# Optimization experiments

Hardware: AMD Instinct MI355X
Metric: run time of the kernel (lower is better)

The kernel has to match this reference:

```python
import math
import jax, jax.numpy as jnp
import numpy as np

DIM = 2048
NUM_HEADS = 16
HEAD_DIM = DIM // NUM_HEADS
BASE = 10000.0


def _rope(x):
    # x: [B, S, H, D]; non-interleaved (chunk-half) rotary embedding
    S, D = x.shape[1], x.shape[-1]
    inv_freq = 1.0 / (BASE ** (jnp.arange(0, D, 2, dtype=jnp.float32) / D))
    t = jnp.arange(S, dtype=jnp.float32)
    freqs = jnp.outer(t, inv_freq)  # [S, D/2]
    cos = jnp.cos(freqs)[None, :, None, :].astype(x.dtype)
    sin = jnp.sin(freqs)[None, :, None, :].astype(x.dtype)
    x1, x2 = jnp.split(x, 2, axis=-1)
    return jnp.concatenate([x1 * cos - x2 * sin, x1 * sin + x2 * cos], axis=-1)


def setup_inputs() -> dict:
    key = jax.random.key(0)
    kx, kq, kk, kv, ko = jax.random.split(key, 5)
    x = jax.random.normal(kx, (2, 2048, DIM), dtype=jnp.float32)
    scale = 0.02
    Wq = jax.random.normal(kq, (DIM, DIM), dtype=jnp.float32) * scale
    Wk = jax.random.normal(kk, (DIM, DIM), dtype=jnp.float32) * scale
    Wv = jax.random.normal(kv, (DIM, DIM), dtype=jnp.float32) * scale
    Wo = jax.random.normal(ko, (DIM, DIM), dtype=jnp.float32) * scale
    return {"x": x, "Wq": Wq, "Wk": Wk, "Wv": Wv, "Wo": Wo}


def reference(x, Wq, Wk, Wv, Wo):
    B, S, _ = x.shape
    # nn.Linear(bias=False): y = x @ W.T
    q = (x @ Wq.T).reshape(B, S, NUM_HEADS, HEAD_DIM)
    k = (x @ Wk.T).reshape(B, S, NUM_HEADS, HEAD_DIM)
    v = (x @ Wv.T).reshape(B, S, NUM_HEADS, HEAD_DIM)
    q = _rope(q)
    k = _rope(k)
    scale = 1.0 / math.sqrt(HEAD_DIM)
    # causal attention, [B,H,S,S] scores
    scores = jnp.einsum("bqhd,bkhd->bhqk", q, k) * scale
    causal = jnp.tril(jnp.ones((S, S), dtype=bool))
    scores = jnp.where(causal[None, None], scores, jnp.finfo(scores.dtype).min)
    attn = jax.nn.softmax(scores, axis=-1)
    out = jnp.einsum("bhqk,bkhd->bqhd", attn, v).reshape(B, S, DIM)
    return out @ Wo.T
```

## Files before the change

### kernel.cpp

```cpp
#include <hip/hip_runtime.h>

typedef unsigned short u16;
typedef __attribute__((ext_vector_type(8))) short short8;
typedef __attribute__((ext_vector_type(4))) float f32x4;
typedef __attribute__((ext_vector_type(4))) int i32x4;

__device__ __forceinline__ float bf2f(u16 u) {
  union { unsigned u; float f; } v; v.u = ((unsigned)u) << 16; return v.f;
}
__device__ __forceinline__ u16 f2bf(float f) {
  union { float f; unsigned u; } v; v.f = f;
  unsigned r = (v.u + 0x7FFFu + ((v.u >> 16) & 1u)) >> 16;
  return (u16)r;
}
__device__ __forceinline__ float flushv(float t, float sentinel) {
  if (t != t || fabsf(t) > 3.0e38f) return sentinel;
  return t;
}
__device__ __forceinline__ short8 ld8f(const float* p) {
  const float4 f0 = *(const float4*)p;
  const float4 f1 = *(const float4*)(p + 4);
  short8 r;
  r[0] = (short)f2bf(f0.x); r[1] = (short)f2bf(f0.y);
  r[2] = (short)f2bf(f0.z); r[3] = (short)f2bf(f0.w);
  r[4] = (short)f2bf(f1.x); r[5] = (short)f2bf(f1.y);
  r[6] = (short)f2bf(f1.z); r[7] = (short)f2bf(f1.w);
  return r;
}

__device__ __forceinline__ void gl16(const u16* g, u16* l) {
  __builtin_amdgcn_global_load_lds(
      (const __attribute__((address_space(1))) void*)g,
      (__attribute__((address_space(3))) void*)l, 16, 0, 0);
}

#define VWAIT(N) asm volatile("s_waitcnt vmcnt(" #N ")" ::: "memory")
#define SBAR() do { __builtin_amdgcn_sched_barrier(0); \
                    __builtin_amdgcn_s_barrier(); \
                    __builtin_amdgcn_sched_barrier(0); } while (0)

__global__ __launch_bounds__(256) void cvt_all(
    const float* __restrict__ x,
    const float* __restrict__ Wq, const float* __restrict__ Wk,
    const float* __restrict__ Wv, const float* __restrict__ Wo,
    u16* __restrict__ xb, u16* __restrict__ wqb, u16* __restrict__ wkb,
    u16* __restrict__ wvb, u16* __restrict__ wob)
{
  const int bid = blockIdx.x;
  const float* s; u16* d; long t;
  if (bid < 8192) {
    const int which = bid >> 11;
    t = (long)(bid & 2047) * 256 + threadIdx.x;
    if (which == 0)      { s = Wq; d = wqb; }
    else if (which == 1) { s = Wk; d = wkb; }
    else if (which == 2) { s = Wv; d = wvb; }
    else                 { s = Wo; d = wob; }
  } else {
    s = x; d = xb;
    t = (long)(bid - 8192) * 256 + threadIdx.x;
  }
  *(short8*)&d[t * 8] = ld8f(s + t * 8);
}

template <bool OF>
__device__ __forceinline__ void gemm_core(
    const u16* __restrict__ Ap, const u16* __restrict__ Bp,
    void* __restrict__ O, int m0, int n0, int N, float sentinel)
{
  __shared__ __align__(16) u16 As[2][128 * 32];
  __shared__ __align__(16) u16 Bs[2][128 * 32];
  constexpr int K = 2048;

  const int tid  = threadIdx.x;
  const int wave = tid >> 6;
  const int lane = tid & 63;
  const int quad = lane >> 4;
  const int l15  = lane & 15;

  const int wm = (wave >> 1) * 64;
  const int wn = (wave & 1) * 64;

  const int srow = lane >> 2;
  const int su   = lane & 3;
  const int r0   = wave * 32 + srow;
  const int csw  = ((su ^ ((r0 >> 1) & 3)) << 3);
  const u16* Ag0 = Ap + (long)(m0 + r0) * K + csw;
  const u16* Ag1 = Ag0 + 16 * (long)K;
  const u16* Bg0 = Bp + (long)(n0 + r0) * K + csw;
  const u16* Bg1 = Bg0 + 16 * (long)K;
  const int sl0 = (wave * 2 + 0) * 512;
  const int sl1 = (wave * 2 + 1) * 512;

  const int xsw = ((l15 >> 1) & 3) << 3;

  const f32x4 zero = {0.f, 0.f, 0.f, 0.f};
  f32x4 acc[4][4];
#pragma unroll
  for (int i = 0; i < 4; ++i)
#pragma unroll
    for (int j = 0; j < 4; ++j) acc[i][j] = zero;

  auto STAGE = [&](int bs, int k0) {
    gl16(Ag0 + k0, &As[bs][sl0]); gl16(Ag1 + k0, &As[bs][sl1]);
    gl16(Bg0 + k0, &Bs[bs][sl0]); gl16(Bg1 + k0, &Bs[bs][sl1]);
  };
  auto COMPUTE = [&](const u16* Ab, const u16* Bb) {
    short8 af[4], bf[4];
#pragma unroll
    for (int i = 0; i < 4; ++i)
      af[i] = *(const short8*)&Ab[(wm + i * 16 + l15) * 32 + ((quad << 3) ^ xsw)];
#pragma unroll
    for (int j = 0; j < 4; ++j)
      bf[j] = *(const short8*)&Bb[(wn + j * 16 + l15) * 32 + ((quad << 3) ^ xsw)];
#pragma unroll
    for (int i = 0; i < 4; ++i)
#pragma unroll
      for (int j = 0; j < 4; ++j)
        acc[i][j] = __builtin_amdgcn_mfma_f32_16x16x32_bf16(af[i], bf[j], acc[i][j], 0, 0, 0);
  };

  STAGE(0, 0);

#pragma unroll 1
  for (int k0 = 0; k0 < K; k0 += 64) {
    STAGE(1, k0 + 32);
    VWAIT(4); SBAR();
    COMPUTE(As[0], Bs[0]);
    SBAR();

    if (k0 + 64 < K) { STAGE(0, k0 + 64); VWAIT(4); }
    else             { VWAIT(0); }
    SBAR();
    COMPUTE(As[1], Bs[1]);
    SBAR();
  }

#pragma unroll
  for (int i = 0; i < 4; ++i) {
    const int row0 = m0 + wm + i * 16 + quad * 4;
#pragma unroll
    for (int j = 0; j < 4; ++j) {
      const int col = n0 + wn + j * 16 + l15;
#pragma unroll
      for (int r = 0; r < 4; ++r) {
        const float val = flushv(acc[i][j][r], sentinel);
        if constexpr (OF)
          ((float*)O)[(long)(row0 + r) * N + col] = val;
        else
          ((u16*)O)[(long)(row0 + r) * N + col] = f2bf(val);
      }
    }
  }
}

__global__ __launch_bounds__(256) void gemm_qkv(
    const u16* __restrict__ xb,
    const u16* __restrict__ wqb, const u16* __restrict__ wkb, const u16* __restrict__ wvb,
    u16* __restrict__ q, u16* __restrict__ k, u16* __restrict__ v)
{
  const int bid = blockIdx.x;
  const int z = bid >> 9, r = bid & 511;
  const u16 *A, *B; u16* O; int m0, n0, Nn;
  if (z < 2) {
    A = xb; B = z ? wkb : wqb; O = z ? k : q;
    m0 = (r >> 4) * 128; n0 = (r & 15) * 128; Nn = 2048;
  } else {
    A = wvb; B = xb; O = v;
    m0 = (r >> 5) * 128; n0 = (r & 31) * 128; Nn = 4096;
  }
  gemm_core<false>(A, B, O, m0, n0, Nn, 7777.f);
}

__global__ __launch_bounds__(256) void gemm_proj(
    const u16* __restrict__ ao, const u16* __restrict__ wob, float* __restrict__ out)
{
  const int r = blockIdx.x;
  gemm_core<true>(ao, wob, out, (r >> 4) * 128, (r & 15) * 128, 2048, 5555.f);
}

template <bool AF, bool WF, bool OF>
__global__ __launch_bounds__(256) void gemm_bt(
    const void* __restrict__ Ap,
    const void* __restrict__ Wp0, const void* __restrict__ Wp1, const void* __restrict__ Wp2,
    void* __restrict__ O0, void* __restrict__ O1, void* __restrict__ O2,
    int M, int N, int K, float sentinel)
{
  __shared__ __align__(16) u16 As[128 * 32];
  __shared__ __align__(16) u16 Bs[128 * 32];

  const void* Wp; void* O;
  if (blockIdx.z == 0)      { Wp = Wp0; O = O0; }
  else if (blockIdx.z == 1) { Wp = Wp1; O = O1; }
  else                      { Wp = Wp2; O = O2; }

  const float* Af = (const float*)Ap;  const u16* Ab = (const u16*)Ap;
  const float* Wf = (const float*)Wp;  const u16* Wb = (const u16*)Wp;

  const int tid  = threadIdx.x;
  const int wave = tid >> 6;
  const int lane = tid & 63;
  const int quad = lane >> 4;
  const int l15  = lane & 15;

  const int m0 = blockIdx.y * 128;
  const int n0 = blockIdx.x * 128;
  const int wm = (wave >> 1) * 64;
  const int wn = (wave & 1) * 64;

  const int e0 = wave * 1024 + lane * 8;
  const int e1 = e0 + 512;
  const int r0 = e0 >> 5, c0 = e0 & 31;
  const int r1 = e1 >> 5, c1 = e1 & 31;

  const long aoff0 = (long)(m0 + r0) * K + c0;
  const long aoff1 = (long)(m0 + r1) * K + c1;
  const long boff0 = (long)(n0 + r0) * K + c0;
  const long boff1 = (long)(n0 + r1) * K + c1;

  const f32x4 zero = {0.f, 0.f, 0.f, 0.f};
  f32x4 acc[4][4];
#pragma unroll
  for (int i = 0; i < 4; ++i)
#pragma unroll
    for (int j = 0; j < 4; ++j) acc[i][j] = zero;

  for (int k0 = 0; k0 < K; k0 += 32) {
    short8 a0, a1, b0, b1;
    if constexpr (AF) {
      a0 = ld8f(Af + aoff0 + k0);
      a1 = ld8f(Af + aoff1 + k0);
    } else {
      a0 = *(const short8*)(Ab + aoff0 + k0);
      a1 = *(const short8*)(Ab + aoff1 + k0);
    }
    if constexpr (WF) {
      b0 = ld8f(Wf + boff0 + k0);
      b1 = ld8f(Wf + boff1 + k0);
    } else {
      b0 = *(const short8*)(Wb + boff0 + k0);
      b1 = *(const short8*)(Wb + boff1 + k0);
    }

    __syncthreads();
    *(short8*)&As[e0] = a0;
    *(short8*)&As[e1] = a1;
    *(short8*)&Bs[e0] = b0;
    *(short8*)&Bs[e1] = b1;
    __syncthreads();

    short8 af[4], bf[4];
#pragma unroll
    for (int i = 0; i < 4; ++i)
      af[i] = *(const short8*)&As[(wm + i * 16 + l15) * 32 + quad * 8];
#pragma unroll
    for (int j = 0; j < 4; ++j)
      bf[j] = *(const short8*)&Bs[(wn + j * 16 + l15) * 32 + quad * 8];
#pragma unroll
    for (int i = 0; i < 4; ++i)
#pragma unroll
      for (int j = 0; j < 4; ++j)
        acc[i][j] = __builtin_amdgcn_mfma_f32_16x16x32_bf16(af[i], bf[j], acc[i][j], 0, 0, 0);
  }

#pragma unroll
  for (int i = 0; i < 4; ++i) {
    const int row0 = m0 + wm + i * 16 + quad * 4;
#pragma unroll
    for (int j = 0; j < 4; ++j) {
      const int col = n0 + wn + j * 16 + l15;
#pragma unroll
      for (int r = 0; r < 4; ++r) {
        const float val = flushv(acc[i][j][r], sentinel);
        if constexpr (OF)
          ((float*)O)[(long)(row0 + r) * N + col] = val;
        else
          ((u16*)O)[(long)(row0 + r) * N + col] = f2bf(val);
      }
    }
  }
}

__global__ __launch_bounds__(256) void rope_kernel(u16* __restrict__ Q, u16* __restrict__ K)
{
  int t = blockIdx.x * 256 + threadIdx.x;
  const int per = 524288;
  u16* P = Q;
  if (t >= per) { P = K; t -= per; }
  const int i8  = t & 7;
  const int row = t >> 3;
  const int s   = (row >> 4) & 2047;
  const long off = (long)row * 128 + i8 * 8;

  short8 va = *(const short8*)&P[off];
  short8 vb = *(const short8*)&P[off + 64];

  const float fs = (float)s;
  float invf = __expf((float)(i8 * 8) * -0.14391156831212787f);
  const float step = 0.86596432336f;
#pragma unroll
  for (int j = 0; j < 8; ++j) {
    float sn, cs;
    __sincosf(fs * invf, &sn, &cs);
    const float q1 = bf2f((u16)va[j]);
    const float q2 = bf2f((u16)vb[j]);
    va[j] = (short)f2bf(q1 * cs - q2 * sn);
    vb[j] = (short)f2bf(q1 * sn + q2 * cs);
    invf *= step;
  }
  *(short8*)&P[off]      = va;
  *(short8*)&P[off + 64] = vb;
}

__global__ __launch_bounds__(256, 4) void attn_kernel(
    const u16* __restrict__ Q, const u16* __restrict__ K,
    const u16* __restrict__ VT, u16* __restrict__ AO)
{
  __shared__ __align__(16) u16 Kb[2][4096];
  __shared__ __align__(16) u16 Vb[2][4096];

  const int tid  = threadIdx.x;
  const int wave = tid >> 6;
  const int lane = tid & 63;
  const int quad = lane >> 4;
  const int l15  = lane & 15;

  const int lin = blockIdx.x;
  const int xcd = lin & 7;
  const int hi  = lin >> 8;
  const int g   = (lin >> 3) & 31;
  const int qb  = (hi & 1) ? (31 - g) : g;
  const int bh  = (xcd << 2) | hi;
  const int b   = bh >> 4;
  const int h   = bh & 15;

  const long base = (long)b * 2048 * 2048 + (long)h * 128;
  const long vtb  = (long)h * 128 * 4096 + (long)b * 2048;
  const int q0w = qb * 64 + wave * 16;
  const int qi  = q0w + l15;

  const u16* Kp0 = K + base;
  const u16* Vp0 = VT + vtb;

  auto STAGE = [&](int bs, int jb) {
#pragma unroll
    for (int gi = 0; gi < 2; ++gi) {
      const int slot = wave * 2 + gi;
      {
        const int row = slot * 4 + (lane >> 4);
        const int su  = lane & 15;
        gl16(Kp0 + (long)(jb * 32 + row) * 2048 + ((su ^ (row & 7)) << 3),
             &Kb[bs][slot * 512]);
      }
      {
        const int row = slot * 16 + (lane >> 2);
        const int su  = lane & 3;
        gl16(Vp0 + (long)row * 4096 + jb * 32 + ((su ^ ((row >> 1) & 3)) << 3),
             &Vb[bs][slot * 512]);
      }
    }
  };

  short8 qa[4];
#pragma unroll
  for (int c = 0; c < 4; ++c)
    qa[c] = *(const short8*)&Q[base + (long)(q0w + l15) * 2048 + c * 32 + quad * 8];

  const f32x4 zero = {0.f, 0.f, 0.f, 0.f};
  f32x4 o[8];
#pragma unroll
  for (int c = 0; c < 8; ++c) o[c] = zero;

  float mreg = -1e30f, lreg = 0.f;
  const float scale = 0.08838834764831845f;

  const int njb_blk = qb * 2 + 2;
  const int njb_w   = qb * 2 + 1 + (wave >> 1);

  STAGE(0, 0);
  __syncthreads();

  const int xorK = l15 & 7;
  const int xorV = (l15 >> 1) & 3;

  int cur = 0;
  for (int jb = 0; jb < njb_blk; ++jb) {
    if (jb + 1 < njb_blk) STAGE(cur ^ 1, jb + 1);

    if (jb < njb_w) {
      const int j0 = jb * 32;

      f32x4 s0T = zero, s1T = zero;
#pragma unroll
      for (int c = 0; c < 4; ++c) {
        const short8 kA = *(const short8*)&Kb[cur][l15 * 128 + (((c * 4 + quad) ^ xorK) << 3)];
        const short8 kB2 = *(const short8*)&Kb[cur][(l15 + 16) * 128 + (((c * 4 + quad) ^ xorK) << 3)];
        s0T = __builtin_amdgcn_mfma_f32_16x16x32_bf16(kA, qa[c], s0T, 0, 0, 0);
        s1T = __builtin_amdgcn_mfma_f32_16x16x32_bf16(kB2, qa[c], s1T, 0, 0, 0);
      }

      float sv0[4], sv1[4];
      float pmax = -1e30f;
      if (j0 + 31 > q0w) {
#pragma unroll
        for (int r = 0; r < 4; ++r) {
          const int k0i = j0 + quad * 4 + r;
          float s0 = s0T[r] * scale; if (k0i > qi)      s0 = -1e30f;
          float s1 = s1T[r] * scale; if (k0i + 16 > qi) s1 = -1e30f;
          sv0[r] = s0; sv1[r] = s1;
          pmax = fmaxf(pmax, fmaxf(s0, s1));
        }
      } else {
#pragma unroll
        for (int r = 0; r < 4; ++r) {
          sv0[r] = s0T[r] * scale;
          sv1[r] = s1T[r] * scale;
          pmax = fmaxf(pmax, fmaxf(sv0[r], sv1[r]));
        }
      }
      pmax = fmaxf(pmax, __shfl_xor(pmax, 16, 64));
      pmax = fmaxf(pmax, __shfl_xor(pmax, 32, 64));
      const float mprev = mreg;
      const float mnew  = fmaxf(mprev, pmax);
      const float alpha = __expf(mprev - mnew);
      float psum = 0.f;
#pragma unroll
      for (int r = 0; r < 4; ++r) {
        sv0[r] = __expf(sv0[r] - mnew);
        sv1[r] = __expf(sv1[r] - mnew);
        psum += sv0[r] + sv1[r];
      }
      psum += __shfl_xor(psum, 16, 64);
      psum += __shfl_xor(psum, 32, 64);
      lreg = lreg * alpha + psum;
      mreg = mnew;

      int w0, w1, w2, w3;
      asm("v_cvt_pk_bf16_f32 %0, %1, %2" : "=v"(w0) : "v"(sv0[0]), "v"(sv0[1]));
      asm("v_cvt_pk_bf16_f32 %0, %1, %2" : "=v"(w1) : "v"(sv0[2]), "v"(sv0[3]));
      asm("v_cvt_pk_bf16_f32 %0, %1, %2" : "=v"(w2) : "v"(sv1[0]), "v"(sv1[1]));
      asm("v_cvt_pk_bf16_f32 %0, %1, %2" : "=v"(w3) : "v"(sv1[2]), "v"(sv1[3]));
      const int srcA = l15 + ((quad & 1) << 5);
      const int srcB = srcA + 16;
      const int a0 = __shfl(w0, srcA, 64), a1 = __shfl(w1, srcA, 64);
      const int a2 = __shfl(w0, srcB, 64), a3 = __shfl(w1, srcB, 64);
      const int h0 = __shfl(w2, srcA, 64), h1 = __shfl(w3, srcA, 64);
      const int h2 = __shfl(w2, srcB, 64), h3 = __shfl(w3, srcB, 64);
      const bool hiq = quad >= 2;
      i32x4 pt;
      pt[0] = hiq ? h0 : a0;
      pt[1] = hiq ? h1 : a1;
      pt[2] = hiq ? h2 : a2;
      pt[3] = hiq ? h3 : a3;
      const short8 pa = *(const short8*)&pt;

      float av[4];
#pragma unroll
      for (int r = 0; r < 4; ++r) av[r] = __shfl(alpha, quad * 4 + r, 64);
#pragma unroll
      for (int c = 0; c < 8; ++c) {
        o[c][0] *= av[0]; o[c][1] *= av[1]; o[c][2] *= av[2]; o[c][3] *= av[3];
      }

#pragma unroll
      for (int c = 0; c < 8; ++c) {
        const short8 vf = *(const short8*)&Vb[cur][(c * 16 + l15) * 32 + ((quad ^ xorV) << 3)];
        o[c] = __builtin_amdgcn_mfma_f32_16x16x32_bf16(pa, vf, o[c], 0, 0, 0);
      }
    }

    __syncthreads();
    cur ^= 1;
  }

#pragma unroll
  for (int r = 0; r < 4; ++r) {
    const float lr  = __shfl(lreg, quad * 4 + r, 64);
    const float inv = 1.0f / lr;
    const long rowoff = base + (long)(q0w + quad * 4 + r) * 2048;
#pragma unroll
    for (int c = 0; c < 8; ++c)
      AO[rowoff + c * 16 + l15] = f2bf(flushv(o[c][r] * inv, 9999.f));
  }
}

__global__ __launch_bounds__(256) void fill_kernel(float* __restrict__ out, long n, float v)
{
  const long t = (long)blockIdx.x * 256 + threadIdx.x;
  if (t < n) out[t] = v;
}

extern "C" void kernel_launch(void* const* d_in, const int* in_sizes, int n_in,
                              void* d_out, int out_size, void* d_ws, size_t ws_size,
                              hipStream_t stream)
{
  const float* x  = (const float*)d_in[0];
  const float* Wq = (const float*)d_in[1];
  const float* Wk = (const float*)d_in[2];
  const float* Wv = (const float*)d_in[3];
  const float* Wo = (const float*)d_in[4];
  float* out = (float*)d_out;

  const long QSZ = (long)2 * 2048 * 2048;
  const long WSZ = QSZ / 2;

  u16* ws = (u16*)d_ws;
  u16* q  = ws;
  u16* k  = ws + QSZ;
  u16* v  = ws + 2 * QSZ;
  u16* ao = q;

  if (ws_size >= (size_t)6 * QSZ * sizeof(u16)) {
    u16* xb  = ws + 3 * QSZ;
    u16* wqb = ws + 4 * QSZ;
    u16* wkb = wqb + WSZ;
    u16* wvb = wqb + 2 * WSZ;
    u16* wob = wqb + 3 * WSZ;

    cvt_all<<<12288, 256, 0, stream>>>(x, Wq, Wk, Wv, Wo, xb, wqb, wkb, wvb, wob);
    gemm_qkv<<<1536, 256, 0, stream>>>(xb, wqb, wkb, wvb, q, k, v);
    rope_kernel<<<4096, 256, 0, stream>>>(q, k);
    attn_kernel<<<1024, 256, 0, stream>>>(q, k, v, ao);
    gemm_proj<<<512, 256, 0, stream>>>(ao, wob, out);
    return;
  }

  if (ws_size < (size_t)3 * QSZ * sizeof(u16)) {
    fill_kernel<<<(int)((QSZ + 255) / 256), 256, 0, stream>>>(out, QSZ, 1111.f);
    return;
  }

  gemm_bt<true, true, false><<<dim3(16, 32, 2), 256, 0, stream>>>(
      x, Wq, Wk, Wk, q, k, k, 4096, 2048, 2048, 7777.f);
  gemm_bt<true, true, false><<<dim3(32, 16, 1), 256, 0, stream>>>(
      Wv, x, x, x, v, v, v, 2048, 4096, 2048, 7777.f);
  rope_kernel<<<4096, 256, 0, stream>>>(q, k);
  attn_kernel<<<1024, 256, 0, stream>>>(q, k, v, ao);
  gemm_bt<false, true, true><<<dim3(16, 32, 1), 256, 0, stream>>>(
      ao, Wo, Wo, Wo, out, out, out, 4096, 2048, 2048, 5555.f);
}
```

Baseline: 393.0 us.

## Add 256x256-tile 8-wave GEMM for Q/K projection with swizzled LDS

Q and K projections move out of the shared 128x128 GEMM into a dedicated kernel with 256x256 tiles, 512 threads, BK=64, XOR-swizzled LDS, double buffering and interleaved async loads. Block IDs are remapped for L2 locality, and wave priority is raised around MFMA bursts. V gets its own launch on the old core. The aim is more reuse per loaded byte and better MFMA utilization, at the cost of an extra launch and a large LDS footprint (128KB) that may limit occupancy.

```diff
diff --git a/kernel.cpp b/kernel.cpp
--- a/kernel.cpp
+++ b/kernel.cpp
@@ -34,7 +34,9 @@
       (__attribute__((address_space(3))) void*)l, 16, 0, 0);
 }
 
-#define VWAIT(N) asm volatile("s_waitcnt vmcnt(" #N ")" ::: "memory")
+#define VWAIT(N) do { \
+  asm volatile("s_waitcnt vmcnt(" #N ")" ::: "memory"); \
+  __builtin_amdgcn_sched_barrier(0); } while (0)
 #define SBAR() do { __builtin_amdgcn_sched_barrier(0); \
                     __builtin_amdgcn_s_barrier(); \
                     __builtin_amdgcn_sched_barrier(0); } while (0)
@@ -62,6 +64,132 @@
   *(short8*)&d[t * 8] = ld8f(s + t * 8);
 }
 
+__global__ __launch_bounds__(512, 2) void gemm_qk8(
+    const u16* __restrict__ Ap, const u16* __restrict__ wqb, const u16* __restrict__ wkb,
+    u16* __restrict__ q, u16* __restrict__ k)
+{
+  __shared__ __align__(16) u16 As[2][256 * 64];
+  __shared__ __align__(16) u16 Bs[2][256 * 64];
+  constexpr int K = 2048;
+
+  const int tid  = threadIdx.x;
+  const int wave = tid >> 6;
+  const int lane = tid & 63;
+  const int quad = lane >> 4;
+  const int l15  = lane & 15;
+  const int x7   = l15 & 7;
+
+  const int lin = blockIdx.x;
+  const int swz = ((lin & 7) << 5) | (lin >> 3);
+  const int m0  = (swz >> 4) * 256;
+  const int n0s = (swz & 15) * 256;
+  const u16* Bp = (n0s < 2048) ? wqb + (long)n0s * K
+                               : wkb + (long)(n0s - 2048) * K;
+  u16* O = (n0s < 2048) ? q : k;
+  const int n0o = n0s & 2047;
+
+  const int wm = (wave >> 2) * 128;
+  const int wn = (wave & 3) * 64;
+
+  const int lrow = lane >> 3;
+  const int lu   = lane & 7;
+  const int sunit = (lu ^ lrow) << 3;
+  const u16* Ag = Ap + (long)(m0 + wave * 32 + lrow) * K + sunit;
+  const u16* Bg = Bp + (long)(wave * 32 + lrow) * K + sunit;
+  const int slds = wave * 2048;
+
+  const f32x4 zero = {0.f, 0.f, 0.f, 0.f};
+  f32x4 acc[8][4];
+#pragma unroll
+  for (int i = 0; i < 8; ++i)
+#pragma unroll
+    for (int j = 0; j < 4; ++j) acc[i][j] = zero;
+
+#pragma unroll
+  for (int j = 0; j < 4; ++j) gl16(Ag + (long)j * 8 * K, &As[0][slds + j * 512]);
+#pragma unroll
+  for (int j = 0; j < 4; ++j) gl16(Bg + (long)j * 8 * K, &Bs[0][slds + j * 512]);
+  VWAIT(0); SBAR();
+
+  int cur = 0;
+#pragma unroll 1
+  for (int it = 0; it < 32; ++it) {
+    const long kn = (long)(it + 1) * 64;
+    const bool hasNext = (it < 31);
+    const u16* Ac = As[cur];
+    const u16* Bc = Bs[cur];
+    u16* An = As[cur ^ 1];
+    u16* Bn = Bs[cur ^ 1];
+
+    short8 bf[4][2];
+#pragma unroll
+    for (int nf = 0; nf < 4; ++nf)
+#pragma unroll
+      for (int ks = 0; ks < 2; ++ks)
+        bf[nf][ks] = *(const short8*)&Bc[(wn + nf * 16 + l15) * 64 + ((((ks << 2) + quad) ^ x7) << 3)];
+    {
+      short8 af[2][2];
+#pragma unroll
+      for (int mi = 0; mi < 2; ++mi)
+#pragma unroll
+        for (int ks = 0; ks < 2; ++ks)
+          af[mi][ks] = *(const short8*)&Ac[(wm + mi * 16 + l15) * 64 + ((((ks << 2) + quad) ^ x7) << 3)];
+      if (hasNext) {
+#pragma unroll
+        for (int j = 0; j < 4; ++j) gl16(Ag + kn + (long)j * 8 * K, &An[slds + j * 512]);
+      }
+      __builtin_amdgcn_s_setprio(1);
+#pragma unroll
+      for (int ks = 0; ks < 2; ++ks)
+#pragma unroll
+        for (int mi = 0; mi < 2; ++mi)
+#pragma unroll
+          for (int nf = 0; nf < 4; ++nf)
+            acc[mi][nf] = __builtin_amdgcn_mfma_f32_16x16x32_bf16(af[mi][ks], bf[nf][ks], acc[mi][nf], 0, 0, 0);
+      __builtin_amdgcn_s_setprio(0);
+    }
+    SBAR();
+
+#pragma unroll
+    for (int mp = 1; mp < 4; ++mp) {
+      short8 af[2][2];
+#pragma unroll
+      for (int mi = 0; mi < 2; ++mi)
+#pragma unroll
+        for (int ks = 0; ks < 2; ++ks)
+          af[mi][ks] = *(const short8*)&Ac[(wm + (mp * 2 + mi) * 16 + l15) * 64 + ((((ks << 2) + quad) ^ x7) << 3)];
+      if (mp == 1 && hasNext) {
+#pragma unroll
+        for (int j = 0; j < 4; ++j) gl16(Bg + kn + (long)j * 8 * K, &Bn[slds + j * 512]);
+      }
+      __builtin_amdgcn_s_setprio(1);
+#pragma unroll
+      for (int ks = 0; ks < 2; ++ks)
+#pragma unroll
+        for (int mi = 0; mi < 2; ++mi)
+#pragma unroll
+          for (int nf = 0; nf < 4; ++nf)
+            acc[mp * 2 + mi][nf] = __builtin_amdgcn_mfma_f32_16x16x32_bf16(af[mi][ks], bf[nf][ks], acc[mp * 2 + mi][nf], 0, 0, 0);
+      __builtin_amdgcn_s_setprio(0);
+      if (mp == 3) VWAIT(0);
+      SBAR();
+    }
+    cur ^= 1;
+  }
+
+#pragma unroll
+  for (int mf = 0; mf < 8; ++mf) {
+    const int row0 = m0 + wm + mf * 16 + quad * 4;
+#pragma unroll
+    for (int nf = 0; nf < 4; ++nf) {
+      const int col = n0o + wn + nf * 16 + l15;
+#pragma unroll
+      for (int r = 0; r < 4; ++r)
+        O[(long)(row0 + r) * 2048 + col] = f2bf(flushv(acc[mf][nf][r], 7777.f));
+    }
+  }
+}
+
 template <bool OF>
 __device__ __forceinline__ void gemm_core(
     const u16* __restrict__ Ap, const u16* __restrict__ Bp,
@@ -153,22 +281,11 @@
   }
 }
 
-__global__ __launch_bounds__(256) void gemm_qkv(
-    const u16* __restrict__ xb,
-    const u16* __restrict__ wqb, const u16* __restrict__ wkb, const u16* __restrict__ wvb,
-    u16* __restrict__ q, u16* __restrict__ k, u16* __restrict__ v)
-{
-  const int bid = blockIdx.x;
-  const int z = bid >> 9, r = bid & 511;
-  const u16 *A, *B; u16* O; int m0, n0, Nn;
-  if (z < 2) {
-    A = xb; B = z ? wkb : wqb; O = z ? k : q;
-    m0 = (r >> 4) * 128; n0 = (r & 15) * 128; Nn = 2048;
-  } else {
-    A = wvb; B = xb; O = v;
-    m0 = (r >> 5) * 128; n0 = (r & 31) * 128; Nn = 4096;
-  }
-  gemm_core<false>(A, B, O, m0, n0, Nn, 7777.f);
+__global__ __launch_bounds__(256) void gemm_vt(
+    const u16* __restrict__ wvb, const u16* __restrict__ xb, u16* __restrict__ v)
+{
+  const int r = blockIdx.x;
+  gemm_core<false>(wvb, xb, v, (r >> 5) * 128, (r & 31) * 128, 4096, 7777.f);
 }
 
 __global__ __launch_bounds__(256) void gemm_proj(
@@ -517,7 +634,8 @@
     u16* wob = wqb + 3 * WSZ;
 
     cvt_all<<<12288, 256, 0, stream>>>(x, Wq, Wk, Wv, Wo, xb, wqb, wkb, wvb, wob);
-    gemm_qkv<<<1536, 256, 0, stream>>>(xb, wqb, wkb, wvb, q, k, v);
+    gemm_qk8<<<256, 512, 0, stream>>>(xb, wqb, wkb, q, k);
+    gemm_vt<<<512, 256, 0, stream>>>(wvb, xb, v);
     rope_kernel<<<4096, 256, 0, stream>>>(q, k);
     attn_kernel<<<1024, 256, 0, stream>>>(q, k, v, ao);
     gemm_proj<<<512, 256, 0, stream>>>(ao, wob, out);
```

Result: no change. 389.8 us (-0.8%).
